# Performance work log

Measured on AMD Instinct MI355X. Metric: run time of the kernel, lower is better.

## Reference

```python
import jax, jax.numpy as jnp
import numpy as np

B, T, D = 16, 2048, 1024


def setup_inputs() -> dict:
    key = jax.random.key(0)
    ks = jax.random.split(key, 7)
    s = 1.0 / np.sqrt(D)  # nn.Linear default init bound
    u = lambda k, shape: jax.random.uniform(k, shape, jnp.float32, -s, s)
    return {
        "x": jax.random.normal(ks[0], (B, T, D), jnp.float32),
        "h0": jnp.zeros((B, D), jnp.float32),
        "W_in": u(ks[1], (2 * D, D)),
        "b_in": u(ks[2], (2 * D,)),
        "W_dt": u(ks[3], (D, D)),
        "b_dt": u(ks[4], (D,)),
        "W_out": u(ks[5], (D, D)),
        "b_out": u(ks[6], (D,)),
    }


def reference(x, h0, W_in, b_in, W_dt, b_dt, W_out, b_out):
    # in_proj then chunk: first half x_part, second half gate
    xz = jnp.einsum("btd,ed->bte", x, W_in) + b_in          # [B,T,2D]
    x_part, gate = jnp.split(xz, 2, axis=-1)                  # each [B,T,D]
    dt = jax.nn.sigmoid(jnp.einsum("btd,ed->bte", x_part, W_dt) + b_dt)  # [B,T,D]

    def step(h, inp):
        dt_t, xp_t = inp                                      # [B,D] each
        h = (1.0 - dt_t) * h + dt_t * xp_t                    # gated EMA update
        return h, h

    _, hs = jax.lax.scan(step, h0,
                         (jnp.swapaxes(dt, 0, 1), jnp.swapaxes(x_part, 0, 1)))
    hs = jnp.swapaxes(hs, 0, 1)                               # [B,T,D]
    y = jnp.einsum("btd,ed->bte", hs * jax.nn.sigmoid(gate), W_out) + b_out
    return y
```

## Files before the change

kernel.cpp:

```cpp
#include <hip/hip_runtime.h>
#include <hip/hip_bf16.h>
#include <cstdint>

typedef __attribute__((ext_vector_type(8))) short short8;
typedef __attribute__((ext_vector_type(4))) float f32x4;
typedef __attribute__((ext_vector_type(8))) unsigned short ushort8;

#define B_ 16
#define T_ 2048
#define D_ 1024
#define M_ (B_*T_)
#define NC 64
#define CL 32

static __device__ __forceinline__ float bf2f(unsigned short u) {
  unsigned int x = ((unsigned int)u) << 16;
  return __builtin_bit_cast(float, x);
}
static __device__ __forceinline__ unsigned short f2bf(float f) {
  unsigned int x = __builtin_bit_cast(unsigned int, f);
  unsigned int r = x + 0x7fffu + ((x >> 16) & 1u);
  return (unsigned short)(r >> 16);
}
static __device__ __forceinline__ float sigmoidf(float v) {
  return 1.f / (1.f + __expf(-v));
}

typedef const __attribute__((address_space(1))) unsigned int* gas1_t;
typedef __attribute__((address_space(3))) unsigned int* las3_t;
static __device__ __forceinline__ void async_copy16(const void* g, void* l) {
  __builtin_amdgcn_global_load_lds((gas1_t)g, (las3_t)l, 16, 0, 0);
}

#define VMCNT8 asm volatile("s_waitcnt vmcnt(8)" ::: "memory")
#define VMCNT6 asm volatile("s_waitcnt vmcnt(6)" ::: "memory")
#define VMCNT4 asm volatile("s_waitcnt vmcnt(4)" ::: "memory")
#define VMCNT2 asm volatile("s_waitcnt vmcnt(2)" ::: "memory")
#define VMCNT0 asm volatile("s_waitcnt vmcnt(0)" ::: "memory")
#define LGKM0  asm volatile("s_waitcnt lgkmcnt(0)" ::: "memory")
#define SBAR   __builtin_amdgcn_s_barrier()
#define SCHED0 __builtin_amdgcn_sched_barrier(0)

__global__ void cvt_all(const float* __restrict__ x,  unsigned short* __restrict__ xb,
                        const float* __restrict__ w1, unsigned short* __restrict__ o1,
                        const float* __restrict__ w2, unsigned short* __restrict__ o2,
                        const float* __restrict__ w3, unsigned short* __restrict__ o3) {
  long i = (long)blockIdx.x * blockDim.x + threadIdx.x;
  long stride = (long)gridDim.x * blockDim.x;
  for (; i < 4718592; i += stride) {
    const float* src; unsigned short* dst; long off;
    if (i < 4194304)      { src = x;  dst = xb; off = i; }
    else if (i < 4456448) { src = w1; dst = o1; off = i - 4194304; }
    else if (i < 4587520) { src = w2; dst = o2; off = i - 4456448; }
    else                  { src = w3; dst = o3; off = i - 4587520; }
    const float4* p = (const float4*)(src + off * 8);
    float4 a = p[0], b = p[1];
    ushort8 o;
    o[0] = f2bf(a.x); o[1] = f2bf(a.y); o[2] = f2bf(a.z); o[3] = f2bf(a.w);
    o[4] = f2bf(b.x); o[5] = f2bf(b.y); o[6] = f2bf(b.z); o[7] = f2bf(b.w);
    *(ushort8*)(dst + off * 8) = o;
  }
}

template<int EPI>
__global__ __launch_bounds__(512, 2) void gemm256(
    const unsigned short* __restrict__ A, long lda,
    const unsigned short* __restrict__ Bw,
    const float* __restrict__ bias,
    void* __restrict__ Cout, long ldc,
    int nbx)
{
  constexpr int KT = 16;
  __shared__ __align__(16) unsigned short lds[65536];

  const int tid = threadIdx.x;
  const int l  = tid & 63, w = tid >> 6;
  const int wm = w >> 2, wn = w & 3;
  const int fr = l & 15, g = l >> 4;
  const int t8 = tid >> 3;
  const int c8x = ((l & 7) ^ (l >> 3)) << 4;
  const int s0 = ((g ^ (fr & 7)) << 4);
  const int aoff  = wm * 8192 + fr * 128 + s0;
  const int aoff1 = aoff ^ 0x40;
  const int boff  = 65536 + wn * 4096 + fr * 128 + s0;
  const int boff1 = boff ^ 0x40;
  const int tB = (w >> 2) * 64 + (w & 3) * 8 + (l >> 3);

  const int nwg = gridDim.x;
  const int cpx = nwg >> 3;
  const int bid = blockIdx.x;
  const int swz = (bid & 7) * cpx + (bid >> 3);
  const long m0 = (long)(swz / nbx) * 256;
  const long n0 = (long)(swz % nbx) * 256;

  const char* Ab = (const char*)A;
  const char* Bb = (const char*)Bw;
  const long ldab = lda * 2;
  char* LB = (char*)lds;

  auto stA = [&](int kt, int h, int nb) {
    char* lb = LB + nb * 32768 + h * 16384 + w * 1024;
    long col = (long)kt * 128 + c8x;
    async_copy16(Ab + (m0 + h * 64 + t8) * ldab + col, lb);
    async_copy16(Ab + (m0 + 128 + h * 64 + t8) * ldab + col, lb + 8192);
  };
  auto stB = [&](int kt, int h, int nb) {
    char* lb = LB + 65536 + nb * 32768 + h * 16384 + w * 1024;
    long col = (long)kt * 128 + c8x;
    async_copy16(Bb + (n0 + tB + h * 32) * 2048 + col, lb);
    async_copy16(Bb + (n0 + tB + 128 + h * 32) * 2048 + col, lb + 8192);
  };

  f32x4 acc[8][4] = {};
  short8 af[4][2], bf0[2][2], bf1[2][2];

#define RD_A(DST, MH, CUR) do {                                                \
    const char* p0_ = LB + (CUR) * 32768 + (MH) * 16384 + aoff;                \
    const char* p1_ = LB + (CUR) * 32768 + (MH) * 16384 + aoff1;               \
    _Pragma("unroll") for (int mi = 0; mi < 4; ++mi) {                         \
      DST[mi][0] = *(const short8*)(p0_ + mi * 2048);                          \
      DST[mi][1] = *(const short8*)(p1_ + mi * 2048); }                        \
  } while (0)
#define RD_B(DST, NH, CUR) do {                                                \
    const char* p0_ = LB + (CUR) * 32768 + (NH) * 16384 + boff;                \
    const char* p1_ = LB + (CUR) * 32768 + (NH) * 16384 + boff1;               \
    _Pragma("unroll") for (int ni = 0; ni < 2; ++ni) {                         \
      DST[ni][0] = *(const short8*)(p0_ + ni * 2048);                          \
      DST[ni][1] = *(const short8*)(p1_ + ni * 2048); }                        \
  } while (0)
#define MM(AF, BF, MB, NB) do {                                                \
    __builtin_amdgcn_s_setprio(1);                                             \
    _Pragma("unroll") for (int mi = 0; mi < 4; ++mi)                           \
    _Pragma("unroll") for (int ni = 0; ni < 2; ++ni) {                         \
      acc[(MB)+mi][(NB)+ni] = __builtin_amdgcn_mfma_f32_16x16x32_bf16(         \
          AF[mi][0], BF[ni][0], acc[(MB)+mi][(NB)+ni], 0, 0, 0);               \
      acc[(MB)+mi][(NB)+ni] = __builtin_amdgcn_mfma_f32_16x16x32_bf16(         \
          AF[mi][1], BF[ni][1], acc[(MB)+mi][(NB)+ni], 0, 0, 0); }             \
    __builtin_amdgcn_s_setprio(0);                                             \
  } while (0)

  stA(0, 0, 0); stB(0, 0, 0); stB(0, 1, 0); stA(0, 1, 0);
  VMCNT4; SCHED0; SBAR;

  for (int t = 0; t < KT; ++t) {
    const int cur = t & 1, nxt = cur ^ 1;
    const bool nl = (t + 1 < KT);
    RD_A(af, 0, cur); RD_B(bf0, 0, cur); SCHED0;
    if (nl) { stA(t + 1, 0, nxt); stB(t + 1, 0, nxt); } SCHED0;
    SBAR; LGKM0; SCHED0;
    MM(af, bf0, 0, 0);
    if (nl) { VMCNT6; } else { VMCNT2; }
    SCHED0; SBAR; SCHED0;
    RD_B(bf1, 1, cur); SCHED0;
    if (nl) { stB(t + 1, 1, nxt); stA(t + 1, 1, nxt); } SCHED0;
    SBAR; LGKM0; SCHED0;
    MM(af, bf1, 0, 2);
    if (nl) { VMCNT8; } else { VMCNT0; }
    SCHED0; SBAR; SCHED0;
    RD_A(af, 1, cur); SCHED0;
    SBAR; LGKM0; SCHED0;
    MM(af, bf0, 4, 0);
    MM(af, bf1, 4, 2);
    if (nl) { VMCNT4; }
    SCHED0; SBAR; SCHED0;
  }
#undef RD_A
#undef RD_B
#undef MM

  __syncthreads();

  char* ep = LB + w * 16384;
  const int rq = l >> 4;
  if (EPI != 2) {
#pragma unroll
    for (int mi = 0; mi < 8; ++mi)
#pragma unroll
      for (int ni = 0; ni < 4; ++ni) {
        int cl = ni * 16 + fr;
        float bv = bias[n0 + wn * 64 + cl];
#pragma unroll
        for (int r = 0; r < 4; ++r) {
          float v = acc[mi][ni][r] + bv;
          if (EPI == 1) v = sigmoidf(v);
          int row = mi * 16 + rq * 4 + r;
          int byte = (row * 128 + cl * 2) ^ ((row & 7) << 4);
          *(unsigned short*)(ep + byte) = f2bf(v);
        }
      }
    LGKM0; SCHED0;
#pragma unroll
    for (int i = 0; i < 16; ++i) {
      int row = i * 8 + (l >> 3);
      int cb = (l & 7) * 16;
      int byte = (row * 128 + cb) ^ ((row & 7) << 4);
      short8 v = *(const short8*)(ep + byte);
      *(short8*)((unsigned short*)Cout + (m0 + wm * 128 + row) * ldc
                 + n0 + wn * 64 + (cb >> 1)) = v;
    }
  } else {
#pragma unroll
    for (int p = 0; p < 2; ++p) {
#pragma unroll
      for (int mi = 0; mi < 4; ++mi)
#pragma unroll
        for (int ni = 0; ni < 4; ++ni) {
          int cl = ni * 16 + fr;
          float bv = bias[n0 + wn * 64 + cl];
#pragma unroll
          for (int r = 0; r < 4; ++r) {
            float v = acc[p * 4 + mi][ni][r] + bv;
            int row = mi * 16 + rq * 4 + r;
            int byte = (row * 256 + cl * 4) ^ ((row & 7) << 4);
            *(float*)(ep + byte) = v;
          }
        }
      LGKM0; SCHED0;
#pragma unroll
      for (int i = 0; i < 16; ++i) {
        int row = i * 4 + (l >> 4);
        int cb = (l & 15) * 16;
        int byte = (row * 256 + cb) ^ ((row & 7) << 4);
        f32x4 v = *(const f32x4*)(ep + byte);
        *(f32x4*)((float*)Cout + (m0 + wm * 128 + p * 64 + row) * ldc
                  + n0 + wn * 64 + (cb >> 2)) = v;
      }
      LGKM0; SCHED0;
    }
  }
}

__global__ void scan_passA(const unsigned short* __restrict__ dtb,
                           const unsigned short* __restrict__ xz,
                           float* __restrict__ P, float* __restrict__ Hl)
{
  int idx = blockIdx.x * blockDim.x + threadIdx.x;
  int d8 = idx & 127;
  int c  = (idx >> 7) & (NC - 1);
  int b  = idx >> 13;
  int d0 = d8 * 8;
  long mbase = (long)b * T_ + (long)c * CL;
  float h[8] = {0,0,0,0,0,0,0,0};
  float p[8] = {1,1,1,1,1,1,1,1};
#pragma unroll 4
  for (int t = 0; t < CL; ++t) {
    long m = mbase + t;
    ushort8 dv = *(const ushort8*)(dtb + m * D_ + d0);
    ushort8 xv = *(const ushort8*)(xz + m * (2 * D_) + d0);
#pragma unroll
    for (int j = 0; j < 8; ++j) {
      float dt = bf2f(dv[j]);
      float xp = bf2f(xv[j]);
      float om = 1.f - dt;
      h[j] = om * h[j] + dt * xp;
      p[j] *= om;
    }
  }
  long pb = ((long)(b * NC + c)) * D_ + d0;
#pragma unroll
  for (int j = 0; j < 8; ++j) { P[pb + j] = p[j]; Hl[pb + j] = h[j]; }
}

__global__ void scan_passC(unsigned short* dts,
                           const unsigned short* __restrict__ xz,
                           const float* __restrict__ h0,
                           const float* __restrict__ P,
                           const float* __restrict__ Hl)
{
  int idx = blockIdx.x * blockDim.x + threadIdx.x;
  int d8 = idx & 127;
  int c  = (idx >> 7) & (NC - 1);
  int b  = idx >> 13;
  int d0 = d8 * 8;
  long mbase = (long)b * T_ + (long)c * CL;

  float h[8];
#pragma unroll
  for (int j = 0; j < 8; ++j) h[j] = h0[(long)b * D_ + d0 + j];

  for (int jc = 0; jc < c; ++jc) {
    long pb = ((long)(b * NC + jc)) * D_ + d0;
    float pj[8], hj[8];
    *(f32x4*)&pj[0] = *(const f32x4*)(P + pb);
    *(f32x4*)&pj[4] = *(const f32x4*)(P + pb + 4);
    *(f32x4*)&hj[0] = *(const f32x4*)(Hl + pb);
    *(f32x4*)&hj[4] = *(const f32x4*)(Hl + pb + 4);
#pragma unroll
    for (int j = 0; j < 8; ++j) h[j] = hj[j] + pj[j] * h[j];
  }

#pragma unroll 4
  for (int t = 0; t < CL; ++t) {
    long m = mbase + t;
    ushort8 dv = *(const ushort8*)(dts + m * D_ + d0);
    ushort8 xv = *(const ushort8*)(xz + m * (2 * D_) + d0);
    ushort8 gv = *(const ushort8*)(xz + m * (2 * D_) + D_ + d0);
    ushort8 ov;
#pragma unroll
    for (int j = 0; j < 8; ++j) {
      float dt = bf2f(dv[j]);
      float xp = bf2f(xv[j]);
      h[j] = (1.f - dt) * h[j] + dt * xp;
      float gt = bf2f(gv[j]);
      ov[j] = f2bf(h[j] * sigmoidf(gt));
    }
    *(ushort8*)(dts + m * D_ + d0) = ov;
  }
}

extern "C" void kernel_launch(void* const* d_in, const int* in_sizes, int n_in,
                              void* d_out, int out_size, void* d_ws, size_t ws_size,
                              hipStream_t stream) {
  const float* x     = (const float*)d_in[0];
  const float* h0    = (const float*)d_in[1];
  const float* W_in  = (const float*)d_in[2];
  const float* b_in  = (const float*)d_in[3];
  const float* W_dt  = (const float*)d_in[4];
  const float* b_dt  = (const float*)d_in[5];
  const float* W_out = (const float*)d_in[6];
  const float* b_out = (const float*)d_in[7];
  float* out = (float*)d_out;

  char* ws = (char*)d_ws;
  const size_t OFF_XB    = 0;
  const size_t OFF_WIN   = 67108864;
  const size_t OFF_WDT   = 71303168;
  const size_t OFF_WOUT  = 73400320;
  const size_t OFF_XZ    = 75497472;
  const size_t OFF_DTS   = 209715200;
  const size_t NEEDED    = 281018368;
  if (ws_size < NEEDED) return;

  unsigned short* xb    = (unsigned short*)(ws + OFF_XB);
  unsigned short* wbin  = (unsigned short*)(ws + OFF_WIN);
  unsigned short* wbdt  = (unsigned short*)(ws + OFF_WDT);
  unsigned short* wbout = (unsigned short*)(ws + OFF_WOUT);
  unsigned short* xz    = (unsigned short*)(ws + OFF_XZ);
  unsigned short* dts   = (unsigned short*)(ws + OFF_DTS);
  float* P  = (float*)(ws + OFF_XB);
  float* Hl = (float*)(ws + OFF_XB + 4194304);

  cvt_all<<<2048, 256, 0, stream>>>(x, xb, W_in, wbin, W_dt, wbdt, W_out, wbout);

  gemm256<0><<<(M_/256)*(2*D_/256), 512, 0, stream>>>(xb, D_, wbin, b_in, xz, 2*D_, 2*D_/256);
  gemm256<1><<<(M_/256)*(D_/256), 512, 0, stream>>>(xz, 2*D_, wbdt, b_dt, dts, D_, D_/256);
  scan_passA<<<512, 256, 0, stream>>>(dts, xz, P, Hl);
  scan_passC<<<512, 256, 0, stream>>>(dts, xz, h0, P, Hl);
  gemm256<2><<<(M_/256)*(D_/256), 512, 0, stream>>>(dts, D_, wbout, b_out, out, D_, D_/256);
}
```

Measured before the change: 432.4 us.

## Fuse fp32-to-bf16 conversion of x into the input projection GEMM loader

Drops the separate pass that converts x to bf16. The first GEMM now loads fp32 x straight into registers, rounds it to bf16 and writes it into LDS, while the weight-only conversion kernel stays. This removes a full write and re-read of a 64 MB bf16 copy of x. In exchange, A-tile loads go through registers instead of async LDS copies and the loop waits for all loads each iteration, so latency hiding and register pressure in that GEMM get worse.

```diff
diff --git a/kernel.cpp b/kernel.cpp
--- a/kernel.cpp
+++ b/kernel.cpp
@@ -41,30 +41,26 @@
 #define SBAR   __builtin_amdgcn_s_barrier()
 #define SCHED0 __builtin_amdgcn_sched_barrier(0)
 
-__global__ void cvt_all(const float* __restrict__ x,  unsigned short* __restrict__ xb,
-                        const float* __restrict__ w1, unsigned short* __restrict__ o1,
-                        const float* __restrict__ w2, unsigned short* __restrict__ o2,
-                        const float* __restrict__ w3, unsigned short* __restrict__ o3) {
+__global__ void cvt_w(const float* __restrict__ w1, unsigned short* __restrict__ o1,
+                      const float* __restrict__ w2, unsigned short* __restrict__ o2,
+                      const float* __restrict__ w3, unsigned short* __restrict__ o3) {
   long i = (long)blockIdx.x * blockDim.x + threadIdx.x;
-  long stride = (long)gridDim.x * blockDim.x;
-  for (; i < 4718592; i += stride) {
-    const float* src; unsigned short* dst; long off;
-    if (i < 4194304)      { src = x;  dst = xb; off = i; }
-    else if (i < 4456448) { src = w1; dst = o1; off = i - 4194304; }
-    else if (i < 4587520) { src = w2; dst = o2; off = i - 4456448; }
-    else                  { src = w3; dst = o3; off = i - 4587520; }
-    const float4* p = (const float4*)(src + off * 8);
-    float4 a = p[0], b = p[1];
-    ushort8 o;
-    o[0] = f2bf(a.x); o[1] = f2bf(a.y); o[2] = f2bf(a.z); o[3] = f2bf(a.w);
-    o[4] = f2bf(b.x); o[5] = f2bf(b.y); o[6] = f2bf(b.z); o[7] = f2bf(b.w);
-    *(ushort8*)(dst + off * 8) = o;
-  }
-}
-
-template<int EPI>
+  const float* src; unsigned short* dst; long off;
+  if (i < 262144)      { src = w1; dst = o1; off = i; }
+  else if (i < 393216) { src = w2; dst = o2; off = i - 262144; }
+  else                 { src = w3; dst = o3; off = i - 393216; }
+  const float4* p = (const float4*)(src + off * 8);
+  float4 a = p[0], b = p[1];
+  ushort8 o;
+  o[0] = f2bf(a.x); o[1] = f2bf(a.y); o[2] = f2bf(a.z); o[3] = f2bf(a.w);
+  o[4] = f2bf(b.x); o[5] = f2bf(b.y); o[6] = f2bf(b.z); o[7] = f2bf(b.w);
+  *(ushort8*)(dst + off * 8) = o;
+}
+
+template<int EPI, int AF32>
 __global__ __launch_bounds__(512, 2) void gemm256(
     const unsigned short* __restrict__ A, long lda,
+    const float* __restrict__ Axf,
     const unsigned short* __restrict__ Bw,
     const float* __restrict__ bias,
     void* __restrict__ Cout, long ldc,
@@ -109,6 +105,30 @@
     long col = (long)kt * 128 + c8x;
     async_copy16(Bb + (n0 + tB + h * 32) * 2048 + col, lb);
     async_copy16(Bb + (n0 + tB + 128 + h * 32) * 2048 + col, lb + 8192);
+  };
+  auto ldA32 = [&](int kt, float4* xr) {
+    const float* base = Axf + (m0 + t8) * 1024 + kt * 64 + (c8x >> 1);
+    xr[0] = *(const float4*)(base);
+    xr[1] = *(const float4*)(base + 4);
+    xr[2] = *(const float4*)(base + 131072);
+    xr[3] = *(const float4*)(base + 131072 + 4);
+    xr[4] = *(const float4*)(base + 65536);
+    xr[5] = *(const float4*)(base + 65536 + 4);
+    xr[6] = *(const float4*)(base + 196608);
+    xr[7] = *(const float4*)(base + 196608 + 4);
+  };
+  auto pk2 = [&](float4 a, float4 b) {
+    ushort8 o;
+    o[0] = f2bf(a.x); o[1] = f2bf(a.y); o[2] = f2bf(a.z); o[3] = f2bf(a.w);
+    o[4] = f2bf(b.x); o[5] = f2bf(b.y); o[6] = f2bf(b.z); o[7] = f2bf(b.w);
+    return o;
+  };
+  auto wrA32 = [&](int nb, const float4* xr) {
+    char* d = LB + nb * 32768 + w * 1024 + l * 16;
+    *(ushort8*)(d)         = pk2(xr[0], xr[1]);
+    *(ushort8*)(d + 8192)  = pk2(xr[2], xr[3]);
+    *(ushort8*)(d + 16384) = pk2(xr[4], xr[5]);
+    *(ushort8*)(d + 24576) = pk2(xr[6], xr[7]);
   };
 
   f32x4 acc[8][4] = {};
@@ -139,30 +159,59 @@
     __builtin_amdgcn_s_setprio(0);                                             \
   } while (0)
 
-  stA(0, 0, 0); stB(0, 0, 0); stB(0, 1, 0); stA(0, 1, 0);
-  VMCNT4; SCHED0; SBAR;
+  if constexpr (AF32) {
+    float4 xr[8];
+    ldA32(0, xr);
+    stB(0, 0, 0); stB(0, 1, 0);
+    wrA32(0, xr);
+    VMCNT0; LGKM0; SCHED0; SBAR;
+  } else {
+    stA(0, 0, 0); stB(0, 0, 0); stB(0, 1, 0); stA(0, 1, 0);
+    VMCNT4; SCHED0; SBAR;
+  }
 
   for (int t = 0; t < KT; ++t) {
     const int cur = t & 1, nxt = cur ^ 1;
     const bool nl = (t + 1 < KT);
-    RD_A(af, 0, cur); RD_B(bf0, 0, cur); SCHED0;
-    if (nl) { stA(t + 1, 0, nxt); stB(t + 1, 0, nxt); } SCHED0;
-    SBAR; LGKM0; SCHED0;
-    MM(af, bf0, 0, 0);
-    if (nl) { VMCNT6; } else { VMCNT2; }
-    SCHED0; SBAR; SCHED0;
-    RD_B(bf1, 1, cur); SCHED0;
-    if (nl) { stB(t + 1, 1, nxt); stA(t + 1, 1, nxt); } SCHED0;
-    SBAR; LGKM0; SCHED0;
-    MM(af, bf1, 0, 2);
-    if (nl) { VMCNT8; } else { VMCNT0; }
-    SCHED0; SBAR; SCHED0;
-    RD_A(af, 1, cur); SCHED0;
-    SBAR; LGKM0; SCHED0;
-    MM(af, bf0, 4, 0);
-    MM(af, bf1, 4, 2);
-    if (nl) { VMCNT4; }
-    SCHED0; SBAR; SCHED0;
+    if constexpr (AF32) {
+      float4 xr[8];
+      RD_A(af, 0, cur); RD_B(bf0, 0, cur); SCHED0;
+      if (nl) { ldA32(t + 1, xr); stB(t + 1, 0, nxt); } SCHED0;
+      SBAR; LGKM0; SCHED0;
+      MM(af, bf0, 0, 0);
+      SCHED0; SBAR; SCHED0;
+      RD_B(bf1, 1, cur); SCHED0;
+      if (nl) { stB(t + 1, 1, nxt); } SCHED0;
+      SBAR; LGKM0; SCHED0;
+      MM(af, bf1, 0, 2);
+      SCHED0; SBAR; SCHED0;
+      RD_A(af, 1, cur); SCHED0;
+      if (nl) { wrA32(nxt, xr); } SCHED0;
+      SBAR; LGKM0; SCHED0;
+      MM(af, bf0, 4, 0);
+      MM(af, bf1, 4, 2);
+      if (nl) { VMCNT0; }
+      SCHED0; SBAR; SCHED0;
+    } else {
+      RD_A(af, 0, cur); RD_B(bf0, 0, cur); SCHED0;
+      if (nl) { stA(t + 1, 0, nxt); stB(t + 1, 0, nxt); } SCHED0;
+      SBAR; LGKM0; SCHED0;
+      MM(af, bf0, 0, 0);
+      if (nl) { VMCNT6; } else { VMCNT2; }
+      SCHED0; SBAR; SCHED0;
+      RD_B(bf1, 1, cur); SCHED0;
+      if (nl) { stB(t + 1, 1, nxt); stA(t + 1, 1, nxt); } SCHED0;
+      SBAR; LGKM0; SCHED0;
+      MM(af, bf1, 0, 2);
+      if (nl) { VMCNT8; } else { VMCNT0; }
+      SCHED0; SBAR; SCHED0;
+      RD_A(af, 1, cur); SCHED0;
+      SBAR; LGKM0; SCHED0;
+      MM(af, bf0, 4, 0);
+      MM(af, bf1, 4, 2);
+      if (nl) { VMCNT4; }
+      SCHED0; SBAR; SCHED0;
+    }
   }
 #undef RD_A
 #undef RD_B
@@ -322,7 +371,7 @@
   float* out = (float*)d_out;
 
   char* ws = (char*)d_ws;
-  const size_t OFF_XB    = 0;
+  const size_t OFF_PH    = 0;
   const size_t OFF_WIN   = 67108864;
   const size_t OFF_WDT   = 71303168;
   const size_t OFF_WOUT  = 73400320;
@@ -331,20 +380,22 @@
   const size_t NEEDED    = 281018368;
   if (ws_size < NEEDED) return;
 
-  unsigned short* xb    = (unsigned short*)(ws + OFF_XB);
   unsigned short* wbin  = (unsigned short*)(ws + OFF_WIN);
   unsigned short* wbdt  = (unsigned short*)(ws + OFF_WDT);
   unsigned short* wbout = (unsigned short*)(ws + OFF_WOUT);
   unsigned short* xz    = (unsigned short*)(ws + OFF_XZ);
   unsigned short* dts   = (unsigned short*)(ws + OFF_DTS);
-  float* P  = (float*)(ws + OFF_XB);
-  float* Hl = (float*)(ws + OFF_XB + 4194304);
-
-  cvt_all<<<2048, 256, 0, stream>>>(x, xb, W_in, wbin, W_dt, wbdt, W_out, wbout);
-
-  gemm256<0><<<(M_/256)*(2*D_/256), 512, 0, stream>>>(xb, D_, wbin, b_in, xz, 2*D_, 2*D_/256);
-  gemm256<1><<<(M_/256)*(D_/256), 512, 0, stream>>>(xz, 2*D_, wbdt, b_dt, dts, D_, D_/256);
+  float* P  = (float*)(ws + OFF_PH);
+  float* Hl = (float*)(ws + OFF_PH + 4194304);
+
+  cvt_w<<<2048, 256, 0, stream>>>(W_in, wbin, W_dt, wbdt, W_out, wbout);
+
+  gemm256<0, 1><<<(M_/256)*(2*D_/256), 512, 0, stream>>>(
+      nullptr, D_, x, wbin, b_in, xz, 2*D_, 2*D_/256);
+  gemm256<1, 0><<<(M_/256)*(D_/256), 512, 0, stream>>>(
+      xz, 2*D_, nullptr, wbdt, b_dt, dts, D_, D_/256);
   scan_passA<<<512, 256, 0, stream>>>(dts, xz, P, Hl);
   scan_passC<<<512, 256, 0, stream>>>(dts, xz, h0, P, Hl);
-  gemm256<2><<<(M_/256)*(D_/256), 512, 0, stream>>>(dts, D_, wbout, b_out, out, D_, D_/256);
-}
+  gemm256<2, 0><<<(M_/256)*(D_/256), 512, 0, stream>>>(
+      dts, D_, nullptr, wbout, b_out, out, D_, D_/256);
+}
```

Result: slower. 498.3 us (+15.2%).
